# Kernel optimization log

Measured on AMD Instinct MI355X. Metric: run time of the kernel, lower is better.

Reference implementation:

```python
import jax, jax.numpy as jnp
import numpy as np

D = 512        # latent_dim
CD = D // 2    # complex_dim = 256
R = 8          # low-rank
UD = 32        # u_dim
NY = 50        # n_y = 2*num_prod + num_inj
SEL_IN = D + UD + 1
H = 128
EPS = 1e-5


def _bn_relu(x, g, b):
    # BatchNorm1d (training mode: batch stats, biased var) + ReLU
    mu = jnp.mean(x, axis=0)
    var = jnp.mean((x - mu) ** 2, axis=0)
    return jax.nn.relu((x - mu) / jnp.sqrt(var + EPS) * g + b)


_LAYERS = [("0", SEL_IN, H), ("1", H, H), ("2", H, D),
           ("a", D, CD), ("o", D, CD),
           ("Ur", D, CD * R), ("Ui", D, CD * R),
           ("Vr", D, CD * R), ("Vi", D, CD * R),
           ("Br", D, CD * UD), ("Bi", D, CD * UD),
           ("Cr", D, NY * CD), ("Ci", D, NY * CD),
           ("D", D, NY * UD)]


def setup_inputs() -> dict:
    key = jax.random.key(0)
    B = 2048
    inp = {}
    k0, k1, k2, kp = jax.random.split(key, 4)
    inp["zt"] = jax.random.normal(k0, (B, D), jnp.float32)
    inp["dt"] = jax.random.uniform(k1, (B, 1), jnp.float32)
    inp["ut"] = jax.random.normal(k2, (B, UD), jnp.float32)
    ks = jax.random.split(kp, len(_LAYERS))
    for (name, fin, fout), k in zip(_LAYERS, ks):
        kw, kb = jax.random.split(k)
        inp["W" + name] = jax.random.normal(kw, (fin, fout), jnp.float32) * 0.02
        inp["b" + name] = jax.random.normal(kb, (fout,), jnp.float32) * 0.02
    # BN affine params for the two hidden selector layers
    inp["g0"] = jnp.ones((H,), jnp.float32)
    inp["be0"] = jnp.zeros((H,), jnp.float32)
    inp["g1"] = jnp.ones((H,), jnp.float32)
    inp["be1"] = jnp.zeros((H,), jnp.float32)
    return inp


def _fwd(zt, dt, ut, W0, b0, g0, be0, W1, b1, g1, be1, W2, b2,
         Wa, ba, Wo, bo, WUr, bUr, WUi, bUi, WVr, bVr, WVi, bVi,
         WBr, bBr, WBi, bBi, WCr, bCr, WCi, bCi, WD, bD):
    B = zt.shape[0]
    z = jax.lax.complex(zt[:, :CD], zt[:, CD:])               # [B, CD] complex
    x = jnp.concatenate([zt, ut, dt], axis=-1)                # [B, SEL_IN]
    h = _bn_relu(x @ W0 + b0, g0, be0)
    h = _bn_relu(h @ W1 + b1, g1, be1)
    hz = h @ W2 + b2                                          # [B, D]

    alpha = -jax.nn.softplus(hz @ Wa + ba)                    # [B, CD]
    omega = hz @ Wo + bo
    Lam = jnp.exp(jax.lax.complex(alpha, omega))              # |Lam| < 1

    U = jax.lax.complex(hz @ WUr + bUr, hz @ WUi + bUi).reshape(B, CD, R)
    V = jax.lax.complex(hz @ WVr + bVr, hz @ WVi + bVi).reshape(B, CD, R)
    # U (V^H z): [B, CD]
    t = jnp.einsum('bdr,bd->br', jnp.conj(V), z)
    low_rank = jnp.einsum('bdr,br->bd', U, t)

    Bt = jax.lax.complex(hz @ WBr + bBr, hz @ WBi + bBi).reshape(B, CD, UD)
    ut_dt = ut * dt                                           # [B, UD] real
    ut_dt_c = ut_dt.astype(Lam.dtype)
    z_next = Lam * z + low_rank + jnp.einsum('bdu,bu->bd', Bt, ut_dt_c)

    Ct = jax.lax.complex(hz @ WCr + bCr, hz @ WCi + bCi).reshape(B, NY, CD)
    Dt = (hz @ WD + bD).reshape(B, NY, UD)
    yt = jnp.einsum('bnd,bd->bn', Ct, z_next).real + jnp.einsum('bnu,bu->bn', Dt, ut_dt)

    z_next_real = jnp.concatenate([z_next.real, z_next.imag], axis=-1)  # [B, D]
    return z_next_real, yt


def reference(zt, dt, ut, W0, b0, g0, be0, W1, b1, g1, be1, W2, b2,
              Wa, ba, Wo, bo, WUr, bUr, WUi, bUi, WVr, bVr, WVi, bVi,
              WBr, bBr, WBi, bBi, WCr, bCr, WCi, bCi, WD, bD):
    return _fwd(zt, dt, ut, W0, b0, g0, be0, W1, b1, g1, be1, W2, b2,
                Wa, ba, Wo, bo, WUr, bUr, WUi, bUi, WVr, bVr, WVi, bVi,
                WBr, bBr, WBi, bBi, WCr, bCr, WCi, bCi, WD, bD)
```

## Files before the change

kernel.cpp:

```cpp
#include <hip/hip_runtime.h>
#include <hip/hip_bf16.h>
#include <cstdint>
#include <cstddef>


typedef __bf16 bf16;
typedef __bf16 bf16x8 __attribute__((ext_vector_type(8)));
typedef __bf16 bf16x4 __attribute__((ext_vector_type(4)));
typedef float f32x4 __attribute__((ext_vector_type(4)));

__device__ __forceinline__ void async16(const void* g, void* l) {
  __builtin_amdgcn_global_load_lds((const __attribute__((address_space(1))) void*)g,
                                   (__attribute__((address_space(3))) void*)l, 16, 0, 0);
}

__device__ __forceinline__ bool tile_map(int NT, int& m0, int& n0) {
  int L = blockIdx.x;
  int x = L & 7, s = L >> 3;
  int nt = ((s >> 4) << 3) + x;
  if (nt >= NT) return false;
  n0 = nt << 7;
  m0 = (s & 15) << 7;
  return true;
}

__device__ __forceinline__ void gemm_core512(const bf16* __restrict__ A,
                                             const bf16* __restrict__ Bw,
                                             int m0, int n0,
                                             bf16* As, bf16* Bs, f32x4 acc[4][4]) {
  const int tid = threadIdx.x;
  const int w = tid >> 6, l = tid & 63;
  const int wm = (w >> 1) << 6, wn = (w & 1) << 6;
  const int fr = l & 15, quad = l >> 4;
#pragma unroll
  for (int mt = 0; mt < 4; ++mt)
#pragma unroll
    for (int nt = 0; nt < 4; ++nt) { f32x4 z = {0.f, 0.f, 0.f, 0.f}; acc[mt][nt] = z; }

  const int c0 = (w << 7) + l, c1 = c0 + 64;
  const int r0 = c0 >> 2, k0 = ((c0 & 3) ^ ((r0 >> 1) & 3)) << 3;
  const int r1 = c1 >> 2, k1 = ((c1 & 3) ^ ((r1 >> 1) & 3)) << 3;
  const bf16* a0 = A + (size_t)(m0 + r0) * 512 + k0;
  const bf16* a1 = A + (size_t)(m0 + r1) * 512 + k1;
  const bf16* b0 = Bw + (size_t)(n0 + r0) * 512 + k0;
  const bf16* b1 = Bw + (size_t)(n0 + r1) * 512 + k1;
  const int ldsb = w << 10;
  const int sw8 = (quad ^ ((fr >> 1) & 3)) << 3;

  auto issue = [&](int kt, int p) {
    bf16* ab = As + p * 4096 + ldsb;
    bf16* bb = Bs + p * 4096 + ldsb;
    async16(a0 + kt, ab);
    async16(a1 + kt, ab + 512);
    async16(b0 + kt, bb);
    async16(b1 + kt, bb + 512);
  };

  issue(0, 0);
#pragma unroll
  for (int it = 0; it < 16; ++it) {
    const int p = it & 1;
    if (it < 15) {
      issue((it + 1) << 5, p ^ 1);
      asm volatile("s_waitcnt vmcnt(4)" ::: "memory");
    } else {
      asm volatile("s_waitcnt vmcnt(0)" ::: "memory");
    }
    asm volatile("s_barrier" ::: "memory");
    const bf16* as = As + p * 4096;
    const bf16* bs = Bs + p * 4096;
    bf16x8 af[4], bfv[4];
#pragma unroll
    for (int mt = 0; mt < 4; ++mt)
      af[mt] = *(const bf16x8*)(as + (wm + mt * 16 + fr) * 32 + sw8);
#pragma unroll
    for (int nt = 0; nt < 4; ++nt)
      bfv[nt] = *(const bf16x8*)(bs + (wn + nt * 16 + fr) * 32 + sw8);
    asm volatile("s_waitcnt lgkmcnt(0)" ::: "memory");
    asm volatile("s_barrier" ::: "memory");
#pragma unroll
    for (int mt = 0; mt < 4; ++mt)
#pragma unroll
      for (int nt = 0; nt < 4; ++nt)
        acc[mt][nt] = __builtin_amdgcn_mfma_f32_16x16x32_bf16(af[mt], bfv[nt], acc[mt][nt], 0, 0, 0);
  }
}

struct TEntry { const float* src; bf16* dst; int N, tile0, ntn; };
struct TArgs { TEntry e[11]; };

__global__ void k_transpose(TArgs a) {
  __shared__ float tile[64][65];
  int t = blockIdx.x;
  int ei = 0;
  while (ei < 10 && t >= a.e[ei + 1].tile0) ++ei;
  const TEntry E = a.e[ei];
  int lt = t - E.tile0;
  int tk = lt / E.ntn, tn = lt - tk * E.ntn;
  int k0 = tk << 6, n0 = tn << 6;
  int tid = threadIdx.x;
#pragma unroll
  for (int i = 0; i < 4; ++i) {
    int idx = tid + i * 256;
    int kk = idx >> 4, c4 = (idx & 15) << 2;
    const float4 v = *(const float4*)(E.src + (size_t)(k0 + kk) * E.N + n0 + c4);
    tile[c4 + 0][kk] = v.x; tile[c4 + 1][kk] = v.y;
    tile[c4 + 2][kk] = v.z; tile[c4 + 3][kk] = v.w;
  }
  __syncthreads();
#pragma unroll
  for (int i = 0; i < 4; ++i) {
    int idx = tid + i * 256;
    int nn = idx >> 4, k4 = (idx & 15) << 2;
    bf16x4 o;
    o[0] = (bf16)tile[nn][k4 + 0]; o[1] = (bf16)tile[nn][k4 + 1];
    o[2] = (bf16)tile[nn][k4 + 2]; o[3] = (bf16)tile[nn][k4 + 3];
    *(bf16x4*)(E.dst + (size_t)(n0 + nn) * 512 + k0 + k4) = o;
  }
}

__global__ void k_prep(const float* ba, const float* bo, const float* bVr, const float* bVi,
                       const float* bBr, const float* bBi, const float* bD,
                       const float* bUr, const float* bUi, const float* bCr, const float* bCi,
                       float* bbigA, float* bbigB, float* bbigC) {
  int i = blockIdx.x * 256 + threadIdx.x;
  if (i < 22656) {
    float v;
    if (i < 256) v = ba[i];
    else if (i < 512) v = bo[i - 256];
    else if (i < 2560) v = bVr[i - 512];
    else if (i < 4608) v = bVi[i - 2560];
    else if (i < 12800) v = bBr[i - 4608];
    else if (i < 20992) v = bBi[i - 12800];
    else if (i < 22592) v = bD[i - 20992];
    else v = 0.f;
    bbigA[i] = v;
  }
  int j = i - 22656;
  if (j >= 0 && j < 4096) bbigB[j] = (j < 2048) ? bUr[j] : bUi[j - 2048];
  int m = i - (22656 + 4096);
  if (m >= 0 && m < 25600) bbigC[m] = (m < 12800) ? bCr[m] : bCi[m - 12800];
}

__global__ void k_lin0(const float* __restrict__ zt, const float* __restrict__ dt,
                       const float* __restrict__ ut, const float* __restrict__ W0,
                       const float* __restrict__ b0, float* __restrict__ s0) {
  int i = blockIdx.x * 256 + threadIdx.x;
  int b = i >> 7, c = i & 127;
  const float* w = W0 + c;
  const float* x = zt + (size_t)b * 512;
  float acc = b0[c];
#pragma unroll 4
  for (int k = 0; k < 512; ++k) acc = fmaf(x[k], w[(size_t)k * 128], acc);
  const float* u = ut + (size_t)b * 32;
#pragma unroll
  for (int k = 0; k < 32; ++k) acc = fmaf(u[k], w[(size_t)(512 + k) * 128], acc);
  acc = fmaf(dt[b], w[(size_t)544 * 128], acc);
  s0[i] = acc;
}

__global__ void k_stats(const float* __restrict__ s, float* __restrict__ mu,
                        float* __restrict__ rstd) {
  int c = blockIdx.x;
  float sm = 0.f, sq = 0.f;
  for (int r = threadIdx.x; r < 2048; r += 256) {
    float v = s[(size_t)r * 128 + c];
    sm += v; sq += v * v;
  }
#pragma unroll
  for (int o = 32; o >= 1; o >>= 1) { sm += __shfl_down(sm, o); sq += __shfl_down(sq, o); }
  __shared__ float red[8];
  int w = threadIdx.x >> 6;
  if ((threadIdx.x & 63) == 0) { red[w] = sm; red[4 + w] = sq; }
  __syncthreads();
  if (threadIdx.x == 0) {
    float S = red[0] + red[1] + red[2] + red[3];
    float Q = red[4] + red[5] + red[6] + red[7];
    float m = S * (1.f / 2048.f);
    float var = Q * (1.f / 2048.f) - m * m;
    mu[c] = m;
    rstd[c] = rsqrtf(var + 1e-5f);
  }
}

__global__ void k_lin1(const float* __restrict__ s0, const float* __restrict__ mu,
                       const float* __restrict__ rstd, const float* __restrict__ g,
                       const float* __restrict__ be, const float* __restrict__ W1,
                       const float* __restrict__ b1, float* __restrict__ s1) {
  int i = blockIdx.x * 256 + threadIdx.x;
  int b = i >> 7, c = i & 127;
  const float* w = W1 + c;
  const float* x = s0 + (size_t)b * 128;
  float acc = b1[c];
#pragma unroll 4
  for (int k = 0; k < 128; ++k) {
    float h = fmaxf(fmaf((x[k] - mu[k]) * rstd[k], g[k], be[k]), 0.f);
    acc = fmaf(h, w[(size_t)k * 128], acc);
  }
  s1[i] = acc;
}

__global__ void k_lin2(const float* __restrict__ s1, const float* __restrict__ mu,
                       const float* __restrict__ rstd, const float* __restrict__ g,
                       const float* __restrict__ be, const float* __restrict__ W2,
                       const float* __restrict__ b2, bf16* __restrict__ hz) {
  int i = blockIdx.x * 256 + threadIdx.x;
  int b = i >> 9, c = i & 511;
  const float* w = W2 + c;
  const float* x = s1 + (size_t)b * 128;
  float acc = b2[c];
#pragma unroll 4
  for (int k = 0; k < 128; ++k) {
    float h = fmaxf(fmaf((x[k] - mu[k]) * rstd[k], g[k], be[k]), 0.f);
    acc = fmaf(h, w[(size_t)k * 512], acc);
  }
  hz[i] = (bf16)acc;
}

__global__ __launch_bounds__(256) void k_gemmA(
    const bf16* __restrict__ hz, const bf16* __restrict__ WT, const float* __restrict__ bias,
    const float* __restrict__ zt, const float* __restrict__ dt, const float* __restrict__ ut,
    float* __restrict__ pa, float* __restrict__ po,
    float* __restrict__ Bzr, float* __restrict__ Bzi,
    float* __restrict__ tbuf, float* __restrict__ ytout) {
  int m0, n0;
  if (!tile_map(177, m0, n0)) return;
  __shared__ __align__(16) bf16 As[8192], Bs[8192];
  f32x4 acc[4][4];
  gemm_core512(hz, WT, m0, n0, As, Bs, acc);
  const int l = threadIdx.x & 63, w = threadIdx.x >> 6;
  const int wm = (w >> 1) << 6, wn = (w & 1) << 6;
  const int fr = l & 15, quad = l >> 4;
  const int ncol = n0 + wn;

  if (n0 < 512) {
    float* dst = (n0 < 256) ? pa : po;
    int cb = ncol - ((n0 < 256) ? 0 : 256);
#pragma unroll
    for (int mt = 0; mt < 4; ++mt)
#pragma unroll
      for (int j = 0; j < 4; ++j) {
        int b = m0 + wm + mt * 16 + quad * 4 + j;
#pragma unroll
        for (int nt = 0; nt < 4; ++nt) {
          int n = ncol + nt * 16 + fr;
          dst[(size_t)b * 256 + (cb + nt * 16 + fr)] = acc[mt][nt][j] + bias[n];
        }
      }
  } else if (n0 < 4608) {
    const bool isVr = n0 < 2560;
#pragma unroll
    for (int mt = 0; mt < 4; ++mt)
#pragma unroll
      for (int j = 0; j < 4; ++j) {
        int b = m0 + wm + mt * 16 + quad * 4 + j;
        float cre = 0.f, cim = 0.f;
#pragma unroll
        for (int nt = 0; nt < 4; ++nt) {
          int n = ncol + nt * 16 + fr;
          float v = acc[mt][nt][j] + bias[n];
          int d = ((n - 512) & 2047) >> 3;
          float zr = zt[(size_t)b * 512 + d], zi = zt[(size_t)b * 512 + 256 + d];
          if (isVr) { cre += v * zr; cim += v * zi; }
          else      { cre += v * zi; cim -= v * zr; }
        }
        cre += __shfl_xor(cre, 8);
        cim += __shfl_xor(cim, 8);
        if ((l & 8) == 0) {
          int r = fr & 7;
          atomicAdd(&tbuf[((size_t)b * 8 + r) * 2 + 0], cre);
          atomicAdd(&tbuf[((size_t)b * 8 + r) * 2 + 1], cim);
        }
      }
  } else if (n0 < 20992) {
    const bool isBr = n0 < 12800;
    float* dst = isBr ? Bzr : Bzi;
#pragma unroll
    for (int mt = 0; mt < 4; ++mt)
#pragma unroll
      for (int j = 0; j < 4; ++j) {
        int b = m0 + wm + mt * 16 + quad * 4 + j;
        float dtb = dt[b];
#pragma unroll
        for (int g = 0; g < 2; ++g) {
          float s = 0.f;
#pragma unroll
          for (int h = 0; h < 2; ++h) {
            int nt = g * 2 + h;
            int n = ncol + nt * 16 + fr;
            int base = (n - 4608) & 8191;
            float v = acc[mt][nt][j] + bias[n];
            s += v * ut[(size_t)b * 32 + (base & 31)];
          }
          s *= dtb;
          s += __shfl_xor(s, 1); s += __shfl_xor(s, 2);
          s += __shfl_xor(s, 4); s += __shfl_xor(s, 8);
          if ((l & 15) == 0) {
            int d = (((ncol + g * 32) - 4608) & 8191) >> 5;
            dst[(size_t)b * 256 + d] = s;
          }
        }
      }
  } else {
#pragma unroll
    for (int mt = 0; mt < 4; ++mt)
#pragma unroll
      for (int j = 0; j < 4; ++j) {
        int b = m0 + wm + mt * 16 + quad * 4 + j;
        float dtb = dt[b];
#pragma unroll
        for (int g = 0; g < 2; ++g) {
          float s = 0.f;
#pragma unroll
          for (int h = 0; h < 2; ++h) {
            int nt = g * 2 + h;
            int n = ncol + nt * 16 + fr;
            int base = n - 20992;
            float v = acc[mt][nt][j] + bias[n];
            s += v * ut[(size_t)b * 32 + (base & 31)];
          }
          s *= dtb;
          s += __shfl_xor(s, 1); s += __shfl_xor(s, 2);
          s += __shfl_xor(s, 4); s += __shfl_xor(s, 8);
          int nn = ((ncol + g * 32) - 20992) >> 5;
          if ((l & 15) == 0 && nn < 50) ytout[(size_t)b * 50 + nn] = s;
        }
      }
  }
}

__global__ __launch_bounds__(256) void k_gemmB(
    const bf16* __restrict__ hz, const bf16* __restrict__ WT, const float* __restrict__ bias,
    const float* __restrict__ tbuf, float* __restrict__ lr) {
  int m0, n0;
  if (!tile_map(32, m0, n0)) return;
  __shared__ __align__(16) bf16 As[8192], Bs[8192];
  f32x4 acc[4][4];
  gemm_core512(hz, WT, m0, n0, As, Bs, acc);
  const int l = threadIdx.x & 63, w = threadIdx.x >> 6;
  const int wm = (w >> 1) << 6, wn = (w & 1) << 6;
  const int fr = l & 15, quad = l >> 4;
  const int ncol = n0 + wn;
  const bool isUr = n0 < 2048;
#pragma unroll
  for (int mt = 0; mt < 4; ++mt)
#pragma unroll
    for (int j = 0; j < 4; ++j) {
      int b = m0 + wm + mt * 16 + quad * 4 + j;
#pragma unroll
      for (int nt = 0; nt < 4; ++nt) {
        int n = ncol + nt * 16 + fr;
        int base = n & 2047;
        int r = base & 7, d = base >> 3;
        float v = acc[mt][nt][j] + bias[n];
        float tre = tbuf[((size_t)b * 8 + r) * 2], tim = tbuf[((size_t)b * 8 + r) * 2 + 1];
        float cre = isUr ? v * tre : -v * tim;
        float cim = isUr ? v * tim :  v * tre;
        cre += __shfl_xor(cre, 1); cre += __shfl_xor(cre, 2); cre += __shfl_xor(cre, 4);
        cim += __shfl_xor(cim, 1); cim += __shfl_xor(cim, 2); cim += __shfl_xor(cim, 4);
        if ((l & 7) == 0) {
          atomicAdd(&lr[((size_t)b * 256 + d) * 2 + 0], cre);
          atomicAdd(&lr[((size_t)b * 256 + d) * 2 + 1], cim);
        }
      }
    }
}

__global__ void k_assembleZ(const float* __restrict__ zt, const float* __restrict__ pa,
                            const float* __restrict__ po, const float* __restrict__ Bzr,
                            const float* __restrict__ Bzi, const float* __restrict__ lr,
                            float* __restrict__ zout, float* __restrict__ znr,
                            float* __restrict__ zni) {
  int i = blockIdx.x * 256 + threadIdx.x;
  int b = i >> 8, d = i & 255;
  float a = pa[i], o = po[i];
  float sp = fmaxf(a, 0.f) + log1pf(expf(-fabsf(a)));
  float mag = expf(-sp);
  float Lr = mag * cosf(o), Li = mag * sinf(o);
  float zr = zt[(size_t)b * 512 + d], zi = zt[(size_t)b * 512 + 256 + d];
  float re = fmaf(Lr, zr, -Li * zi) + Bzr[i] + lr[2 * i];
  float im = fmaf(Lr, zi,  Li * zr) + Bzi[i] + lr[2 * i + 1];
  zout[(size_t)b * 512 + d] = re;
  zout[(size_t)b * 512 + 256 + d] = im;
  znr[i] = re; zni[i] = im;
}

__global__ __launch_bounds__(256) void k_gemmC(
    const bf16* __restrict__ hz, const bf16* __restrict__ WT, const float* __restrict__ bias,
    const float* __restrict__ znr, const float* __restrict__ zni, float* __restrict__ ytout) {
  int m0, n0;
  if (!tile_map(200, m0, n0)) return;
  __shared__ __align__(16) bf16 As[8192], Bs[8192];
  f32x4 acc[4][4];
  gemm_core512(hz, WT, m0, n0, As, Bs, acc);
  const int l = threadIdx.x & 63, w = threadIdx.x >> 6;
  const int wm = (w >> 1) << 6, wn = (w & 1) << 6;
  const int fr = l & 15, quad = l >> 4;
  const int ncol = n0 + wn;
  const bool isCr = n0 < 12800;
  const int nb = ncol - (isCr ? 0 : 12800);
  const int nn = nb >> 8;
#pragma unroll
  for (int mt = 0; mt < 4; ++mt)
#pragma unroll
    for (int j = 0; j < 4; ++j) {
      int b = m0 + wm + mt * 16 + quad * 4 + j;
      float s = 0.f;
#pragma unroll
      for (int nt = 0; nt < 4; ++nt) {
        int n = ncol + nt * 16 + fr;
        int d = (nb + nt * 16 + fr) & 255;
        float v = acc[mt][nt][j] + bias[n];
        s += isCr ? v * znr[(size_t)b * 256 + d] : -(v * zni[(size_t)b * 256 + d]);
      }
      s += __shfl_xor(s, 1); s += __shfl_xor(s, 2);
      s += __shfl_xor(s, 4); s += __shfl_xor(s, 8);
      if ((l & 15) == 0) atomicAdd(&ytout[(size_t)b * 50 + nn], s);
    }
}

extern "C" void kernel_launch(void* const* d_in, const int* in_sizes, int n_in,
                              void* d_out, int out_size, void* d_ws, size_t ws_size,
                              hipStream_t stream) {
  (void)in_sizes; (void)n_in; (void)out_size; (void)ws_size;
  const float* zt  = (const float*)d_in[0];
  const float* dt  = (const float*)d_in[1];
  const float* ut  = (const float*)d_in[2];
  const float* W0  = (const float*)d_in[3];  const float* b0  = (const float*)d_in[4];
  const float* W1  = (const float*)d_in[5];  const float* b1  = (const float*)d_in[6];
  const float* W2  = (const float*)d_in[7];  const float* b2  = (const float*)d_in[8];
  const float* Wa  = (const float*)d_in[9];  const float* ba  = (const float*)d_in[10];
  const float* Wo  = (const float*)d_in[11]; const float* bo  = (const float*)d_in[12];
  const float* WUr = (const float*)d_in[13]; const float* bUr = (const float*)d_in[14];
  const float* WUi = (const float*)d_in[15]; const float* bUi = (const float*)d_in[16];
  const float* WVr = (const float*)d_in[17]; const float* bVr = (const float*)d_in[18];
  const float* WVi = (const float*)d_in[19]; const float* bVi = (const float*)d_in[20];
  const float* WBr = (const float*)d_in[21]; const float* bBr = (const float*)d_in[22];
  const float* WBi = (const float*)d_in[23]; const float* bBi = (const float*)d_in[24];
  const float* WCr = (const float*)d_in[25]; const float* bCr = (const float*)d_in[26];
  const float* WCi = (const float*)d_in[27]; const float* bCi = (const float*)d_in[28];
  const float* WD  = (const float*)d_in[29]; const float* bD  = (const float*)d_in[30];
  const float* g0  = (const float*)d_in[31]; const float* be0 = (const float*)d_in[32];
  const float* g1  = (const float*)d_in[33]; const float* be1 = (const float*)d_in[34];

  char* ws = (char*)d_ws;
  bf16*  WTbig = (bf16*)(ws + 0);
  bf16*  WTU   = (bf16*)(ws + 23199744);
  bf16*  WTC   = (bf16*)(ws + 27394048);
  bf16*  hz    = (bf16*)(ws + 53608448);
  float* s0    = (float*)(ws + 55705600);
  float* s1    = (float*)(ws + 56754176);
  float* mu0   = (float*)(ws + 57802752);
  float* rstd0 = mu0 + 128;
  float* mu1   = mu0 + 256;
  float* rstd1 = mu0 + 384;
  float* bbigA = (float*)(ws + 57804800);
  float* bbigB = (float*)(ws + 57895424);
  float* bbigC = (float*)(ws + 57911808);
  float* pa    = (float*)(ws + 58014208);
  float* po    = (float*)(ws + 60111360);
  float* Bzr   = (float*)(ws + 62208512);
  float* Bzi   = (float*)(ws + 64305664);
  float* tbuf  = (float*)(ws + 66402816);
  float* lr    = (float*)(ws + 66533888);
  float* znr   = (float*)(ws + 70728192);
  float* zni   = (float*)(ws + 72825344);
  float* zout  = (float*)d_out;
  float* ytout = zout + 2048 * 512;

  k_prep<<<205, 256, 0, stream>>>(ba, bo, bVr, bVi, bBr, bBi, bD, bUr, bUi, bCr, bCi,
                                  bbigA, bbigB, bbigC);

  TArgs ta; int tile0 = 0; int idx = 0;
  auto add = [&](const float* src, bf16* dst, int N) {
    int ntn = N >> 6;
    ta.e[idx].src = src; ta.e[idx].dst = dst; ta.e[idx].N = N;
    ta.e[idx].tile0 = tile0; ta.e[idx].ntn = ntn;
    tile0 += ntn * 8; ++idx;
  };
  add(Wa,  WTbig + (size_t)0 * 512,     256);
  add(Wo,  WTbig + (size_t)256 * 512,   256);
  add(WVr, WTbig + (size_t)512 * 512,   2048);
  add(WVi, WTbig + (size_t)2560 * 512,  2048);
  add(WBr, WTbig + (size_t)4608 * 512,  8192);
  add(WBi, WTbig + (size_t)12800 * 512, 8192);
  add(WD,  WTbig + (size_t)20992 * 512, 1600);
  add(WUr, WTU,                         2048);
  add(WUi, WTU + (size_t)2048 * 512,    2048);
  add(WCr, WTC,                         12800);
  add(WCi, WTC + (size_t)12800 * 512,   12800);
  k_transpose<<<tile0, 256, 0, stream>>>(ta);

  hipMemsetAsync(tbuf, 0, 131072, stream);
  hipMemsetAsync(lr, 0, 4194304, stream);

  k_lin0<<<1024, 256, 0, stream>>>(zt, dt, ut, W0, b0, s0);
  k_stats<<<128, 256, 0, stream>>>(s0, mu0, rstd0);
  k_lin1<<<1024, 256, 0, stream>>>(s0, mu0, rstd0, g0, be0, W1, b1, s1);
  k_stats<<<128, 256, 0, stream>>>(s1, mu1, rstd1);
  k_lin2<<<4096, 256, 0, stream>>>(s1, mu1, rstd1, g1, be1, W2, b2, hz);

  k_gemmA<<<184 * 16, 256, 0, stream>>>(hz, WTbig, bbigA, zt, dt, ut,
                                        pa, po, Bzr, Bzi, tbuf, ytout);
  k_gemmB<<<32 * 16, 256, 0, stream>>>(hz, WTU, bbigB, tbuf, lr);
  k_assembleZ<<<2048, 256, 0, stream>>>(zt, pa, po, Bzr, Bzi, lr, zout, znr, zni);
  k_gemmC<<<200 * 16, 256, 0, stream>>>(hz, WTC, bbigC, znr, zni, ytout);
}
```

Measured before the change: 615.5 us.

## Load MFMA fragments directly from global memory, dropping the LDS staging

Replaces the LDS-staged, double-buffered GEMM core with a version where each wave loads its bf16 A/B fragments straight from global memory into registers, with register double-buffering across K steps. This removes the LDS traffic and the two barriers per K iteration, and adds a launch-bounds occupancy hint of 3 blocks. In exchange, each wave re-reads data that its neighbouring waves also load, so global/L2 traffic goes up, and the loads are 16-byte strided rows that may coalesce less well.

New measurement: 906.0 us. +47.2%, slower.

```diff
diff --git a/kernel.cpp b/kernel.cpp
--- a/kernel.cpp
+++ b/kernel.cpp
@@ -8,11 +8,6 @@
 typedef __bf16 bf16x8 __attribute__((ext_vector_type(8)));
 typedef __bf16 bf16x4 __attribute__((ext_vector_type(4)));
 typedef float f32x4 __attribute__((ext_vector_type(4)));
-
-__device__ __forceinline__ void async16(const void* g, void* l) {
-  __builtin_amdgcn_global_load_lds((const __attribute__((address_space(1))) void*)g,
-                                   (__attribute__((address_space(3))) void*)l, 16, 0, 0);
-}
 
 __device__ __forceinline__ bool tile_map(int NT, int& m0, int& n0) {
   int L = blockIdx.x;
@@ -24,65 +19,39 @@
   return true;
 }
 
-__device__ __forceinline__ void gemm_core512(const bf16* __restrict__ A,
-                                             const bf16* __restrict__ Bw,
-                                             int m0, int n0,
-                                             bf16* As, bf16* Bs, f32x4 acc[4][4]) {
-  const int tid = threadIdx.x;
-  const int w = tid >> 6, l = tid & 63;
+__device__ __forceinline__ void gemm_direct(const bf16* __restrict__ A,
+                                            const bf16* __restrict__ Bw,
+                                            int m0, int n0, f32x4 acc[4][4]) {
+  const int l = threadIdx.x & 63, w = threadIdx.x >> 6;
   const int wm = (w >> 1) << 6, wn = (w & 1) << 6;
-  const int fr = l & 15, quad = l >> 4;
+  const int fr = l & 15, q = l >> 4;
+  const bf16* ap = A + (size_t)(m0 + wm + fr) * 512 + (q << 3);
+  const bf16* bp = Bw + (size_t)(n0 + wn + fr) * 512 + (q << 3);
 #pragma unroll
   for (int mt = 0; mt < 4; ++mt)
 #pragma unroll
     for (int nt = 0; nt < 4; ++nt) { f32x4 z = {0.f, 0.f, 0.f, 0.f}; acc[mt][nt] = z; }
-
-  const int c0 = (w << 7) + l, c1 = c0 + 64;
-  const int r0 = c0 >> 2, k0 = ((c0 & 3) ^ ((r0 >> 1) & 3)) << 3;
-  const int r1 = c1 >> 2, k1 = ((c1 & 3) ^ ((r1 >> 1) & 3)) << 3;
-  const bf16* a0 = A + (size_t)(m0 + r0) * 512 + k0;
-  const bf16* a1 = A + (size_t)(m0 + r1) * 512 + k1;
-  const bf16* b0 = Bw + (size_t)(n0 + r0) * 512 + k0;
-  const bf16* b1 = Bw + (size_t)(n0 + r1) * 512 + k1;
-  const int ldsb = w << 10;
-  const int sw8 = (quad ^ ((fr >> 1) & 3)) << 3;
-
-  auto issue = [&](int kt, int p) {
-    bf16* ab = As + p * 4096 + ldsb;
-    bf16* bb = Bs + p * 4096 + ldsb;
-    async16(a0 + kt, ab);
-    async16(a1 + kt, ab + 512);
-    async16(b0 + kt, bb);
-    async16(b1 + kt, bb + 512);
-  };
-
-  issue(0, 0);
-#pragma unroll
-  for (int it = 0; it < 16; ++it) {
-    const int p = it & 1;
-    if (it < 15) {
-      issue((it + 1) << 5, p ^ 1);
-      asm volatile("s_waitcnt vmcnt(4)" ::: "memory");
-    } else {
-      asm volatile("s_waitcnt vmcnt(0)" ::: "memory");
+  bf16x8 af[2][4], bfv[2][4];
+#pragma unroll
+  for (int mt = 0; mt < 4; ++mt) af[0][mt] = *(const bf16x8*)(ap + mt * 8192);
+#pragma unroll
+  for (int nt = 0; nt < 4; ++nt) bfv[0][nt] = *(const bf16x8*)(bp + nt * 8192);
+#pragma unroll
+  for (int kt = 0; kt < 16; ++kt) {
+    const int c = kt & 1, nx = c ^ 1;
+    if (kt < 15) {
+      const int ko = (kt + 1) << 5;
+#pragma unroll
+      for (int mt = 0; mt < 4; ++mt) af[nx][mt] = *(const bf16x8*)(ap + ko + mt * 8192);
+#pragma unroll
+      for (int nt = 0; nt < 4; ++nt) bfv[nx][nt] = *(const bf16x8*)(bp + ko + nt * 8192);
     }
-    asm volatile("s_barrier" ::: "memory");
-    const bf16* as = As + p * 4096;
-    const bf16* bs = Bs + p * 4096;
-    bf16x8 af[4], bfv[4];
 #pragma unroll
     for (int mt = 0; mt < 4; ++mt)
-      af[mt] = *(const bf16x8*)(as + (wm + mt * 16 + fr) * 32 + sw8);
-#pragma unroll
-    for (int nt = 0; nt < 4; ++nt)
-      bfv[nt] = *(const bf16x8*)(bs + (wn + nt * 16 + fr) * 32 + sw8);
-    asm volatile("s_waitcnt lgkmcnt(0)" ::: "memory");
-    asm volatile("s_barrier" ::: "memory");
-#pragma unroll
-    for (int mt = 0; mt < 4; ++mt)
 #pragma unroll
       for (int nt = 0; nt < 4; ++nt)
-        acc[mt][nt] = __builtin_amdgcn_mfma_f32_16x16x32_bf16(af[mt], bfv[nt], acc[mt][nt], 0, 0, 0);
+        acc[mt][nt] = __builtin_amdgcn_mfma_f32_16x16x32_bf16(af[c][mt], bfv[c][nt],
+                                                              acc[mt][nt], 0, 0, 0);
   }
 }
 
@@ -217,7 +186,7 @@
   hz[i] = (bf16)acc;
 }
 
-__global__ __launch_bounds__(256) void k_gemmA(
+__global__ __launch_bounds__(256, 3) void k_gemmA(
     const bf16* __restrict__ hz, const bf16* __restrict__ WT, const float* __restrict__ bias,
     const float* __restrict__ zt, const float* __restrict__ dt, const float* __restrict__ ut,
     float* __restrict__ pa, float* __restrict__ po,
@@ -225,9 +194,8 @@
     float* __restrict__ tbuf, float* __restrict__ ytout) {
   int m0, n0;
   if (!tile_map(177, m0, n0)) return;
-  __shared__ __align__(16) bf16 As[8192], Bs[8192];
   f32x4 acc[4][4];
-  gemm_core512(hz, WT, m0, n0, As, Bs, acc);
+  gemm_direct(hz, WT, m0, n0, acc);
   const int l = threadIdx.x & 63, w = threadIdx.x >> 6;
   const int wm = (w >> 1) << 6, wn = (w & 1) << 6;
   const int fr = l & 15, quad = l >> 4;
@@ -329,14 +297,13 @@
   }
 }
 
-__global__ __launch_bounds__(256) void k_gemmB(
+__global__ __launch_bounds__(256, 3) void k_gemmB(
     const bf16* __restrict__ hz, const bf16* __restrict__ WT, const float* __restrict__ bias,
     const float* __restrict__ tbuf, float* __restrict__ lr) {
   int m0, n0;
   if (!tile_map(32, m0, n0)) return;
-  __shared__ __align__(16) bf16 As[8192], Bs[8192];
   f32x4 acc[4][4];
-  gemm_core512(hz, WT, m0, n0, As, Bs, acc);
+  gemm_direct(hz, WT, m0, n0, acc);
   const int l = threadIdx.x & 63, w = threadIdx.x >> 6;
   const int wm = (w >> 1) << 6, wn = (w & 1) << 6;
   const int fr = l & 15, quad = l >> 4;
@@ -385,14 +352,13 @@
   znr[i] = re; zni[i] = im;
 }
 
-__global__ __launch_bounds__(256) void k_gemmC(
+__global__ __launch_bounds__(256, 3) void k_gemmC(
     const bf16* __restrict__ hz, const bf16* __restrict__ WT, const float* __restrict__ bias,
     const float* __restrict__ znr, const float* __restrict__ zni, float* __restrict__ ytout) {
   int m0, n0;
   if (!tile_map(200, m0, n0)) return;
-  __shared__ __align__(16) bf16 As[8192], Bs[8192];
   f32x4 acc[4][4];
-  gemm_core512(hz, WT, m0, n0, As, Bs, acc);
+  gemm_direct(hz, WT, m0, n0, acc);
   const int l = threadIdx.x & 63, w = threadIdx.x >> 6;
   const int wm = (w >> 1) << 6, wn = (w & 1) << 6;
   const int fr = l & 15, quad = l >> 4;
```

## Give each wave private LDS tiles to drop workgroup barriers in GEMM core

Applied to the files above, without the earlier changes.

Each wave now loads its own 64-row A and B slices into a private LDS region, so the two s_barrier calls per k-step are gone and waves proceed independently. The cost is redundant global loads: A and B slices shared between waves are fetched twice, and LDS use doubles to 64 KB per block, which may lower occupancy. The vmcnt threshold is raised to 8 to match the doubled number of outstanding loads per thread.

Result: slower. 646.8 us (+5.1%).

```diff
diff --git a/kernel.cpp b/kernel.cpp
--- a/kernel.cpp
+++ b/kernel.cpp
@@ -24,36 +24,32 @@
   return true;
 }
 
-__device__ __forceinline__ void gemm_core512(const bf16* __restrict__ A,
-                                             const bf16* __restrict__ Bw,
-                                             int m0, int n0,
-                                             bf16* As, bf16* Bs, f32x4 acc[4][4]) {
+__device__ __forceinline__ void gemm_wp(const bf16* __restrict__ A,
+                                        const bf16* __restrict__ Bw,
+                                        int m0, int n0,
+                                        bf16* lds, f32x4 acc[4][4]) {
   const int tid = threadIdx.x;
   const int w = tid >> 6, l = tid & 63;
   const int wm = (w >> 1) << 6, wn = (w & 1) << 6;
-  const int fr = l & 15, quad = l >> 4;
+  const int fr = l & 15, q = l >> 4;
+  const int lr = l >> 2;
+  const int koff = ((l & 3) ^ ((l >> 3) & 3)) << 3;
+  const bf16* ag = A + (size_t)(m0 + wm + lr) * 512 + koff;
+  const bf16* bg = Bw + (size_t)(n0 + wn + lr) * 512 + koff;
+  bf16* lw = lds + (w << 13);
+  const int sw = (q ^ ((fr >> 1) & 3)) << 3;
+
 #pragma unroll
   for (int mt = 0; mt < 4; ++mt)
 #pragma unroll
     for (int nt = 0; nt < 4; ++nt) { f32x4 z = {0.f, 0.f, 0.f, 0.f}; acc[mt][nt] = z; }
 
-  const int c0 = (w << 7) + l, c1 = c0 + 64;
-  const int r0 = c0 >> 2, k0 = ((c0 & 3) ^ ((r0 >> 1) & 3)) << 3;
-  const int r1 = c1 >> 2, k1 = ((c1 & 3) ^ ((r1 >> 1) & 3)) << 3;
-  const bf16* a0 = A + (size_t)(m0 + r0) * 512 + k0;
-  const bf16* a1 = A + (size_t)(m0 + r1) * 512 + k1;
-  const bf16* b0 = Bw + (size_t)(n0 + r0) * 512 + k0;
-  const bf16* b1 = Bw + (size_t)(n0 + r1) * 512 + k1;
-  const int ldsb = w << 10;
-  const int sw8 = (quad ^ ((fr >> 1) & 3)) << 3;
-
   auto issue = [&](int kt, int p) {
-    bf16* ab = As + p * 4096 + ldsb;
-    bf16* bb = Bs + p * 4096 + ldsb;
-    async16(a0 + kt, ab);
-    async16(a1 + kt, ab + 512);
-    async16(b0 + kt, bb);
-    async16(b1 + kt, bb + 512);
+    bf16* d = lw + (p << 12);
+#pragma unroll
+    for (int i = 0; i < 4; ++i) async16(ag + kt + i * 8192, d + (i << 9));
+#pragma unroll
+    for (int i = 0; i < 4; ++i) async16(bg + kt + i * 8192, d + 2048 + (i << 9));
   };
 
   issue(0, 0);
@@ -62,27 +58,26 @@
     const int p = it & 1;
     if (it < 15) {
       issue((it + 1) << 5, p ^ 1);
-      asm volatile("s_waitcnt vmcnt(4)" ::: "memory");
+      asm volatile("s_waitcnt vmcnt(8)" ::: "memory");
     } else {
       asm volatile("s_waitcnt vmcnt(0)" ::: "memory");
     }
-    asm volatile("s_barrier" ::: "memory");
-    const bf16* as = As + p * 4096;
-    const bf16* bs = Bs + p * 4096;
+    const bf16* ab = lw + (p << 12);
+    const bf16* bb = ab + 2048;
     bf16x8 af[4], bfv[4];
 #pragma unroll
     for (int mt = 0; mt < 4; ++mt)
-      af[mt] = *(const bf16x8*)(as + (wm + mt * 16 + fr) * 32 + sw8);
+      af[mt] = *(const bf16x8*)(ab + (mt * 16 + fr) * 32 + sw);
 #pragma unroll
     for (int nt = 0; nt < 4; ++nt)
-      bfv[nt] = *(const bf16x8*)(bs + (wn + nt * 16 + fr) * 32 + sw8);
+      bfv[nt] = *(const bf16x8*)(bb + (nt * 16 + fr) * 32 + sw);
     asm volatile("s_waitcnt lgkmcnt(0)" ::: "memory");
-    asm volatile("s_barrier" ::: "memory");
 #pragma unroll
     for (int mt = 0; mt < 4; ++mt)
 #pragma unroll
       for (int nt = 0; nt < 4; ++nt)
-        acc[mt][nt] = __builtin_amdgcn_mfma_f32_16x16x32_bf16(af[mt], bfv[nt], acc[mt][nt], 0, 0, 0);
+        acc[mt][nt] = __builtin_amdgcn_mfma_f32_16x16x32_bf16(af[mt], bfv[nt],
+                                                              acc[mt][nt], 0, 0, 0);
   }
 }
 
@@ -225,9 +220,9 @@
     float* __restrict__ tbuf, float* __restrict__ ytout) {
   int m0, n0;
   if (!tile_map(177, m0, n0)) return;
-  __shared__ __align__(16) bf16 As[8192], Bs[8192];
+  __shared__ __align__(16) bf16 lds[32768];
   f32x4 acc[4][4];
-  gemm_core512(hz, WT, m0, n0, As, Bs, acc);
+  gemm_wp(hz, WT, m0, n0, lds, acc);
   const int l = threadIdx.x & 63, w = threadIdx.x >> 6;
   const int wm = (w >> 1) << 6, wn = (w & 1) << 6;
   const int fr = l & 15, quad = l >> 4;
@@ -334,9 +329,9 @@
     const float* __restrict__ tbuf, float* __restrict__ lr) {
   int m0, n0;
   if (!tile_map(32, m0, n0)) return;
-  __shared__ __align__(16) bf16 As[8192], Bs[8192];
+  __shared__ __align__(16) bf16 lds[32768];
   f32x4 acc[4][4];
-  gemm_core512(hz, WT, m0, n0, As, Bs, acc);
+  gemm_wp(hz, WT, m0, n0, lds, acc);
   const int l = threadIdx.x & 63, w = threadIdx.x >> 6;
   const int wm = (w >> 1) << 6, wn = (w & 1) << 6;
   const int fr = l & 15, quad = l >> 4;
@@ -390,9 +385,9 @@
     const float* __restrict__ znr, const float* __restrict__ zni, float* __restrict__ ytout) {
   int m0, n0;
   if (!tile_map(200, m0, n0)) return;
-  __shared__ __align__(16) bf16 As[8192], Bs[8192];
+  __shared__ __align__(16) bf16 lds[32768];
   f32x4 acc[4][4];
-  gemm_core512(hz, WT, m0, n0, As, Bs, acc);
+  gemm_wp(hz, WT, m0, n0, lds, acc);
   const int l = threadIdx.x & 63, w = threadIdx.x >> 6;
   const int wm = (w >> 1) << 6, wn = (w & 1) << 6;
   const int fr = l & 15, quad = l >> 4;
```
